# Performance work log

Measured on AMD Instinct MI355X. Metric: run time of the kernel, lower is better.

The kernel has to match this reference:

```python
import jax, jax.numpy as jnp
import numpy as np

BATCH = 8
NDATA = 8192
NPOINT = 1024
NSAMPLE = 32
RADIUS = 0.2
CFEAT = 64


def setup_inputs() -> dict:
    key = jax.random.key(0)
    k1, k2, k3 = jax.random.split(key, 3)
    new_xyz = jax.random.normal(k1, (BATCH, NPOINT, 3), dtype=jnp.float32)
    xyz = jax.random.normal(k2, (BATCH, NDATA, 3), dtype=jnp.float32)
    points = jax.random.normal(k3, (BATCH, NDATA, CFEAT), dtype=jnp.float32)
    return {"new_xyz": new_xyz, "xyz": xyz, "points": points}


def reference(new_xyz, xyz, points):
    # Pairwise distances from every centroid to every dataset point.
    # delta: [B, P, N, 3]
    delta = xyz[:, None, :, :] - new_xyz[:, :, None, :]
    dist = jnp.linalg.norm(delta, axis=-1)  # [B, P, N]

    # Sort by distance (the original does a full argsort per centroid).
    sorted_idx = jnp.argsort(dist, axis=-1).astype(jnp.int32)  # [B, P, N]
    sorted_d = jnp.take_along_axis(dist, sorted_idx, axis=-1)  # [B, P, N]

    # Nearest point index replaces out-of-radius slots.
    nearest = sorted_idx[:, :, 0:1]  # [B, P, 1]
    radius_idx = jnp.where(sorted_d < RADIUS, sorted_idx, nearest)
    idx = radius_idx[:, :, :NSAMPLE]  # [B, P, S] int32 (ndataset >= nsample)

    # Batched gathers: grouped_xyz [B, P, S, 3], grouped_points [B, P, S, C].
    grouped_xyz = jnp.take_along_axis(
        xyz[:, None, :, :], idx[..., None], axis=2)
    grouped_points = jnp.take_along_axis(
        points[:, None, :, :], idx[..., None], axis=2)
    new_points = jnp.concatenate([grouped_xyz, grouped_points], axis=-1)
    return (new_points, idx, grouped_xyz)
```

## Files before the change

kernel.cpp:

```cpp
#include <hip/hip_runtime.h>
#include <math.h>

typedef unsigned int   u32;
typedef unsigned long long u64;

#define BATCH   8
#define NDATA   8192
#define NPOINT  1024
#define NSAMPLE 32
#define CFEAT   64
#define ROWF    67
#define MAXCAND 128
#define QPB     4
#define NBX     32
#define NBY     32
#define NBK     (NBX*NBY)

#define OUT_IDX (BATCH*NPOINT*NSAMPLE*ROWF)
#define OUT_GX  (OUT_IDX + BATCH*NPOINT*NSAMPLE)

__device__ __forceinline__ float rnbf(float f) {
    u32 b = __float_as_uint(f);
    b += 0x7FFFu + ((b >> 16) & 1u);
    return __uint_as_float(b & 0xFFFF0000u);
}
__device__ __forceinline__ int clampidx(int v) {
    return (v < 0) ? 0 : (v > NDATA-1 ? NDATA-1 : v);
}
__device__ __forceinline__ int lanes_below(u64 m) {
    return __builtin_amdgcn_mbcnt_hi((u32)(m >> 32),
            __builtin_amdgcn_mbcnt_lo((u32)m, 0));
}
__device__ __forceinline__ int cbucket(float v) {
    int c = (int)floorf((v + 4.5f) * 3.5555556f);
    return c < 0 ? 0 : (c > NBX-1 ? NBX-1 : c);
}
__device__ __forceinline__ int key2(float x, float y) {
    return cbucket(x)*NBY + cbucket(y);
}

__global__ __launch_bounds__(1024)
void bin_kernel(const float* __restrict__ xyz,
                float4* __restrict__ wp, u32* __restrict__ wst)
{
    __shared__ u32 cnt[NBK];
    __shared__ u32 wsum[16];
    const int b = blockIdx.x, tid = threadIdx.x;
    const int lane = tid & 63, wv = tid >> 6;
    const float* bx = xyz + (size_t)b * NDATA * 3;

    cnt[tid] = 0;
    __syncthreads();
    for (int p = tid; p < NDATA; p += 1024)
        atomicAdd(&cnt[key2(bx[p*3], bx[p*3+1])], 1u);
    __syncthreads();

    u32 v = cnt[tid];
    u32 s = v;
    #pragma unroll
    for (int off = 1; off < 64; off <<= 1) {
        u32 t = __shfl_up(s, off);
        if (lane >= off) s += t;
    }
    if (lane == 63) wsum[wv] = s;
    __syncthreads();
    if (tid < 16) {
        u32 w = wsum[tid];
        #pragma unroll
        for (int off = 1; off < 16; off <<= 1) {
            u32 t = __shfl_up(w, off);
            if (tid >= off) w += t;
        }
        wsum[tid] = w;
    }
    __syncthreads();
    u32 excl = s - v + (wv ? wsum[wv-1] : 0u);
    wst[b*(NBK+1) + tid] = excl;
    cnt[tid] = excl;
    if (tid == 0) wst[b*(NBK+1) + NBK] = NDATA;
    __syncthreads();

    for (int p = tid; p < NDATA; p += 1024) {
        float x = bx[p*3], y = bx[p*3+1], z = bx[p*3+2];
        u32 pos = atomicAdd(&cnt[key2(x, y)], 1u);
        wp[(size_t)b*NDATA + pos] = make_float4(x, y, z, __uint_as_float((u32)p));
    }
}

__global__ __launch_bounds__(256, 8)
void grouping_kernel(const float* __restrict__ new_xyz,
                     const float* __restrict__ xyz,
                     const float* __restrict__ points,
                     const float4* __restrict__ wp, const u32* __restrict__ wst,
                     float* __restrict__ out, float T)
{
    __shared__ float cand_s[QPB][MAXCAND];
    __shared__ int   cand_i[QPB][MAXCAND];
    __shared__ int   sel[QPB][NSAMPLE];
    __shared__ __align__(16) float st[QPB][8*ROWF];

    const int tid  = threadIdx.x;
    const int wv   = tid >> 6;
    const int lane = tid & 63;
    const int q    = blockIdx.x * QPB + wv;
    const int b    = q >> 10;

    if (lane < NSAMPLE) sel[wv][lane] = 0;

    const float qx = new_xyz[q*3 + 0];
    const float qy = new_xyz[q*3 + 1];
    const float qz = new_xyz[q*3 + 2];
    const float*  bx = xyz + (size_t)b * NDATA * 3;
    const float4* cp = wp  + (size_t)b * NDATA;

    const int bxlo = cbucket(__fsub_rn(qx, 0.2005f));
    const int bxhi = cbucket(__fadd_rn(qx, 0.2005f));
    const int bylo = cbucket(__fsub_rn(qy, 0.2005f));
    const int byhi = cbucket(__fadd_rn(qy, 0.2005f));
    const u32* ws = wst + b*(NBK+1);

    int n = 0;
    for (int c = bxlo; c <= bxhi; ++c) {
        const u32 j0 = ws[c*NBY + bylo];
        const u32 j1 = ws[c*NBY + byhi + 1];
        for (u32 jb = j0; jb < j1; jb += 64) {
            u32 j  = jb + lane;
            bool in = j < j1;
            u32 jj = in ? j : (j1 - 1u);
            float4 vv = cp[jj];
            float dx = __fsub_rn(vv.x, qx);
            float dy = __fsub_rn(vv.y, qy);
            float dz = __fsub_rn(vv.z, qz);
            float d2 = __fadd_rn(__fadd_rn(__fmul_rn(dx,dx), __fmul_rn(dy,dy)),
                                 __fmul_rn(dz,dz));
            bool cc = in && (d2 < T);
            u64 m = __ballot(cc);
            if (cc) {
                int pos = n + lanes_below(m);
                if (pos < MAXCAND) {
                    cand_s[wv][pos] = __fsqrt_rn(d2);
                    cand_i[wv][pos] = (int)__float_as_uint(vv.w);
                }
            }
            n += (int)__popcll(m);
        }
    }

    int mini = 0;
    if (n == 0) {
        float mind = 3.402823466e38f; int mi = 0;
        for (int k = 0; k < NDATA/64; ++k) {
            int i = (k << 6) + lane;
            float dx = __fsub_rn(bx[i*3+0], qx);
            float dy = __fsub_rn(bx[i*3+1], qy);
            float dz = __fsub_rn(bx[i*3+2], qz);
            float d2 = __fadd_rn(__fadd_rn(__fmul_rn(dx,dx), __fmul_rn(dy,dy)),
                                 __fmul_rn(dz,dz));
            if (d2 < mind) { mind = d2; mi = i; }
        }
        float ms = __fsqrt_rn(mind);
        for (int off = 32; off; off >>= 1) {
            float os = __shfl_xor(ms, off);
            int   oi = __shfl_xor(mi, off);
            if (os < ms || (os == ms && oi < mi)) { ms = os; mi = oi; }
        }
        mini = mi;
    }

    __syncthreads();

    const int nj = n > MAXCAND ? MAXCAND : n;
    for (int kk = lane; kk < nj; kk += 64) {
        float sk = cand_s[wv][kk];
        int   ik = cand_i[wv][kk];
        int r = 0;
        for (int mm = 0; mm < nj; ++mm) {
            float sm = cand_s[wv][mm];
            int   im = cand_i[wv][mm];
            r += (int)((sm < sk) | ((sm == sk) & (im < ik)));
        }
        if (r < NSAMPLE) sel[wv][r] = clampidx(ik);
    }
    __syncthreads();
    {
        const int nsel = nj < NSAMPLE ? nj : NSAMPLE;
        if (lane >= nsel && lane < NSAMPLE) {
            int pad = (nj > 0) ? sel[wv][0] : clampidx(mini);
            sel[wv][lane] = pad;
        }
    }
    __syncthreads();

    if (lane < NSAMPLE)
        out[OUT_IDX + (size_t)q*NSAMPLE + lane] = rnbf((float)sel[wv][lane]);

    for (int e = lane; e < NSAMPLE*3; e += 64) {
        int sR = e / 3, c2 = e - sR*3;
        int is = sel[wv][sR];
        out[OUT_GX + (size_t)q*(NSAMPLE*3) + e] = rnbf(bx[is*3 + c2]);
    }

    const float* prow = points + (size_t)b * NDATA * CFEAT;
    float* onp = out + (size_t)q * (NSAMPLE*ROWF);
    const int gq = lane >> 4;
    const int lq = lane & 15;
    for (int g = 0; g < 4; ++g) {
        #pragma unroll
        for (int p = 0; p < 2; ++p) {
            int rl = p*4 + gq;
            int is = sel[wv][g*8 + rl];
            const float4 v = *reinterpret_cast<const float4*>(
                                 prow + (size_t)is*CFEAT + 4*lq);
            float* d = &st[wv][rl*ROWF + 3 + 4*lq];
            d[0] = rnbf(v.x); d[1] = rnbf(v.y); d[2] = rnbf(v.z); d[3] = rnbf(v.w);
        }
        if (lane < 24) {
            int rl = lane / 3, c = lane - rl*3;
            int is = sel[wv][g*8 + rl];
            st[wv][rl*ROWF + c] = rnbf(bx[(size_t)is*3 + c]);
        }
        __syncthreads();
        for (int i = lane; i < 134; i += 64) {
            float4 t = *reinterpret_cast<const float4*>(&st[wv][4*i]);
            *reinterpret_cast<float4*>(onp + (size_t)g*536 + 4*i) = t;
        }
        __syncthreads();
    }
}

extern "C" void kernel_launch(void* const* d_in, const int* in_sizes, int n_in,
                              void* d_out, int out_size, void* d_ws, size_t ws_size,
                              hipStream_t stream) {
    union { u32 u; float f; } lo, hi, mid;
    lo.u = 0u; hi.f = 0.05f;
    while (hi.u - lo.u > 1u) {
        mid.u = lo.u + (hi.u - lo.u) / 2u;
        if (sqrtf(mid.f) >= 0.2f) hi.u = mid.u; else lo.u = mid.u;
    }
    float T = hi.f;

    float4* wp  = (float4*)d_ws;
    u32*    wst = (u32*)(wp + (size_t)BATCH*NDATA);

    const float* nxz = (const float*)d_in[0];
    const float* xyz = (const float*)d_in[1];
    const float* pts = (const float*)d_in[2];

    bin_kernel<<<BATCH, 1024, 0, stream>>>(xyz, wp, wst);
    grouping_kernel<<<(BATCH*NPOINT)/QPB, 256, 0, stream>>>(
        nxz, xyz, pts, wp, wst, (float*)d_out, T);
}
```

Before: 123.2 us.

## Replace block barriers with wave fences, prefetch gathers, use nontemporal stores

Each wave only touches its own shared-memory slice, so the block-wide barriers are replaced with compiler-only memory fences that rely on wave-level execution ordering. The point-feature gathers for the next 8-row group are issued before the current group's LDS staging is written out, overlapping global loads with stores. All output writes use nontemporal stores to avoid polluting caches. Relying on an empty asm fence for LDS ordering within a wave risks hazards if the compiler or hardware reorders LDS accesses.

After: 124.5 us. No clear change (+1.1%).

```diff
diff --git a/kernel.cpp b/kernel.cpp
--- a/kernel.cpp
+++ b/kernel.cpp
@@ -3,6 +3,7 @@
 
 typedef unsigned int   u32;
 typedef unsigned long long u64;
+typedef float nf4 __attribute__((ext_vector_type(4)));
 
 #define BATCH   8
 #define NDATA   8192
@@ -30,6 +31,9 @@
 __device__ __forceinline__ int lanes_below(u64 m) {
     return __builtin_amdgcn_mbcnt_hi((u32)(m >> 32),
             __builtin_amdgcn_mbcnt_lo((u32)m, 0));
+}
+__device__ __forceinline__ void wave_lds_fence() {
+    asm volatile("" ::: "memory");
 }
 __device__ __forceinline__ int cbucket(float v) {
     int c = (int)floorf((v + 4.5f) * 3.5555556f);
@@ -167,7 +171,7 @@
         mini = mi;
     }
 
-    __syncthreads();
+    wave_lds_fence();
 
     const int nj = n > MAXCAND ? MAXCAND : n;
     for (int kk = lane; kk < nj; kk += 64) {
@@ -181,7 +185,7 @@
         }
         if (r < NSAMPLE) sel[wv][r] = clampidx(ik);
     }
-    __syncthreads();
+    wave_lds_fence();
     {
         const int nsel = nj < NSAMPLE ? nj : NSAMPLE;
         if (lane >= nsel && lane < NSAMPLE) {
@@ -189,42 +193,54 @@
             sel[wv][lane] = pad;
         }
     }
-    __syncthreads();
+    wave_lds_fence();
 
     if (lane < NSAMPLE)
-        out[OUT_IDX + (size_t)q*NSAMPLE + lane] = rnbf((float)sel[wv][lane]);
+        __builtin_nontemporal_store(rnbf((float)sel[wv][lane]),
+                                    &out[OUT_IDX + (size_t)q*NSAMPLE + lane]);
 
     for (int e = lane; e < NSAMPLE*3; e += 64) {
         int sR = e / 3, c2 = e - sR*3;
         int is = sel[wv][sR];
-        out[OUT_GX + (size_t)q*(NSAMPLE*3) + e] = rnbf(bx[is*3 + c2]);
+        __builtin_nontemporal_store(rnbf(bx[is*3 + c2]),
+                                    &out[OUT_GX + (size_t)q*(NSAMPLE*3) + e]);
     }
 
     const float* prow = points + (size_t)b * NDATA * CFEAT;
     float* onp = out + (size_t)q * (NSAMPLE*ROWF);
     const int gq = lane >> 4;
     const int lq = lane & 15;
+
+    int isA = sel[wv][gq];
+    int isB = sel[wv][4 + gq];
+    float4 vA = *reinterpret_cast<const float4*>(prow + (size_t)isA*CFEAT + 4*lq);
+    float4 vB = *reinterpret_cast<const float4*>(prow + (size_t)isB*CFEAT + 4*lq);
+
     for (int g = 0; g < 4; ++g) {
-        #pragma unroll
-        for (int p = 0; p < 2; ++p) {
-            int rl = p*4 + gq;
-            int is = sel[wv][g*8 + rl];
-            const float4 v = *reinterpret_cast<const float4*>(
-                                 prow + (size_t)is*CFEAT + 4*lq);
-            float* d = &st[wv][rl*ROWF + 3 + 4*lq];
-            d[0] = rnbf(v.x); d[1] = rnbf(v.y); d[2] = rnbf(v.z); d[3] = rnbf(v.w);
+        {
+            float* d0 = &st[wv][gq*ROWF + 3 + 4*lq];
+            d0[0]=rnbf(vA.x); d0[1]=rnbf(vA.y); d0[2]=rnbf(vA.z); d0[3]=rnbf(vA.w);
+            float* d1 = &st[wv][(4+gq)*ROWF + 3 + 4*lq];
+            d1[0]=rnbf(vB.x); d1[1]=rnbf(vB.y); d1[2]=rnbf(vB.z); d1[3]=rnbf(vB.w);
         }
         if (lane < 24) {
             int rl = lane / 3, c = lane - rl*3;
             int is = sel[wv][g*8 + rl];
             st[wv][rl*ROWF + c] = rnbf(bx[(size_t)is*3 + c]);
         }
-        __syncthreads();
+        wave_lds_fence();
+        if (g < 3) {
+            isA = sel[wv][(g+1)*8 + gq];
+            isB = sel[wv][(g+1)*8 + 4 + gq];
+            vA = *reinterpret_cast<const float4*>(prow + (size_t)isA*CFEAT + 4*lq);
+            vB = *reinterpret_cast<const float4*>(prow + (size_t)isB*CFEAT + 4*lq);
+        }
         for (int i = lane; i < 134; i += 64) {
-            float4 t = *reinterpret_cast<const float4*>(&st[wv][4*i]);
-            *reinterpret_cast<float4*>(onp + (size_t)g*536 + 4*i) = t;
-        }
-        __syncthreads();
+            nf4 t = *reinterpret_cast<const nf4*>(&st[wv][4*i]);
+            __builtin_nontemporal_store(t,
+                reinterpret_cast<nf4*>(onp + (size_t)g*536 + 4*i));
+        }
+        wave_lds_fence();
     }
 }
 
```
